# Optimization experiments

Measured on AMD Instinct MI355X. Metric: run time of the kernel, lower is better.

Reference implementation:

```python
import jax, jax.numpy as jnp
from jax import lax
import numpy as np


def _tv1d_row(y, lam):
    """Condat's direct O(n) 1D TV-L1 prox (TV1D_denoise) on one row.
    Solves min_x 0.5*||x-y||^2 + lam * sum|x_{i+1}-x_i|.
    State machine translation of Condat (2013) Algorithm 1.
    """
    W = y.shape[0]
    idx = jnp.arange(W)
    dt = y.dtype

    def write(out, lo, hi, v):
        # out[lo:hi+1] = v  (masked, jit-friendly)
        return jnp.where((idx >= lo) & (idx <= hi), v, out)

    def cond_fn(s):
        return ~s[9]

    def body_fn(s):
        out, k, k0, km, kp, umin, umax, vmin, vmax, done = s
        T = jnp.array(True)
        F = jnp.array(False)

        def branchA(_):  # k == W-1
            def a1(_):  # umin < 0: flush negative segment at vmin
                o = write(out, k0, km, vmin)
                k0n = km + 1
                vminn = y[jnp.minimum(k0n, W - 1)]
                return (o, k0n, k0n, k0n, kp, lam, vminn + lam - vmax, vminn, vmax, F)

            def a2(_):  # umax > 0: flush positive segment at vmax
                o = write(out, k0, kp, vmax)
                k0n = kp + 1
                vmaxn = y[jnp.minimum(k0n, W - 1)]
                return (o, k0n, k0n, km, k0n, vmaxn - lam - vmin, -lam, vmin, vmaxn, F)

            def a3(_):  # terminate
                v = vmin + umin / (k - k0 + 1).astype(dt)
                o = write(out, k0, k, v)
                return (o, k, k0, km, kp, umin, umax, v, vmax, T)

            return lax.cond(umin < 0, a1,
                            lambda _: lax.cond(umax > 0, a2, a3, None), None)

        def branchB(_):  # k < W-1
            yn = y[jnp.minimum(k + 1, W - 1)]
            umin_t = umin + yn - vmin
            umax_t = umax + yn - vmax

            def b1(_):  # negative jump: flush at vmin, restart
                o = write(out, k0, km, vmin)
                k0n = km + 1
                vminn = y[jnp.minimum(k0n, W - 1)]
                return (o, k0n, k0n, k0n, k0n, lam, -lam, vminn, vminn + 2 * lam, F)

            def b2(_):  # positive jump: flush at vmax, restart
                o = write(out, k0, kp, vmax)
                k0n = kp + 1
                vmaxn = y[jnp.minimum(k0n, W - 1)]
                return (o, k0n, k0n, k0n, k0n, lam, -lam, vmaxn - 2 * lam, vmaxn, F)

            def b3(_):  # extend current segment
                kn = k + 1
                denom = (kn - k0 + 1).astype(dt)
                hit_min = umin_t >= lam
                hit_max = umax_t <= -lam
                vminn = jnp.where(hit_min, vmin + (umin_t - lam) / denom, vmin)
                uminn = jnp.where(hit_min, lam, umin_t)
                kmn = jnp.where(hit_min, kn, km)
                vmaxn = jnp.where(hit_max, vmax + (umax_t + lam) / denom, vmax)
                umaxn = jnp.where(hit_max, -lam, umax_t)
                kpn = jnp.where(hit_max, kn, kp)
                return (out, kn, k0, kmn, kpn, uminn, umaxn, vminn, vmaxn, F)

            return lax.cond(umin_t < -lam, b1,
                            lambda _: lax.cond(umax_t > lam, b2, b3, None), None)

        return lax.cond(k == W - 1, branchA, branchB, None)

    z = jnp.int32(0)
    init = (jnp.zeros_like(y), z, z, z, z, lam, -lam, y[0] - lam, y[0] + lam, jnp.array(False))
    return lax.while_loop(cond_fn, body_fn, init)[0]


def tv1d_batch(y_flat, lam_rows):
    return jax.vmap(_tv1d_row)(y_flat, lam_rows)


def setup_inputs() -> dict:
    key = jax.random.key(0)
    N, C, H, W = 8, 3, 256, 512
    y = jax.random.normal(key, (N, C, H, W), dtype=jnp.float32)
    # learned lmbd parameter initialized so that softplus(lmbd) = 0.5 (lmbd_init=0.5, lmbd_zero<0 -> offset 0)
    lmbd = jnp.full((1, C), float(np.log(np.expm1(0.5))), dtype=jnp.float32)
    return {"y": y, "lmbd": lmbd}


def reference(y, lmbd):
    N, C, H, W = y.shape
    lam = jax.nn.softplus(lmbd)  # get_lmbd_val with lmbd_offset = 0
    lam_rows = jnp.broadcast_to(lam.reshape(1, C, 1), (N, C, H)).reshape(-1)  # (N*C*H,)
    x = tv1d_batch(y.reshape(-1, W), lam_rows)
    return x.reshape(N, C, H, W)
```

## Files before the change

kernel.cpp:

```cpp
#include <hip/hip_runtime.h>
#include <math.h>

#define TVW 512
#define TVH 256
#define TVC 3
#define WPB 2
#define BLOCK (WPB * 64)

__global__ __launch_bounds__(BLOCK)
void tv1d_condat_wave_kernel(const float* __restrict__ y,
                             const float* __restrict__ lmbd,
                             float* __restrict__ out,
                             int total_rows) {
    __shared__ __align__(16) float buf [WPB * TVW + 4];
    __shared__ __align__(16) float bneg[WPB * TVW + 4];
    __shared__ float rtab[520];
    const int tid  = threadIdx.x;
    const int wave = tid >> 6;
    const int lane = tid & 63;
    const bool hi  = lane >= 32;
    const int base_row = blockIdx.x * WPB;
    const int row = base_row + wave;

    {
        float4* b4 = (float4*)buf;
        float4* n4 = (float4*)bneg;
        const float4* s4 = (const float4*)(y + (size_t)base_row * TVW);
        #pragma unroll
        for (int i = 0; i < (WPB * TVW / 4); i += BLOCK) {
            const float4 v = s4[i + tid];
            b4[i + tid] = v;
            n4[i + tid] = make_float4(-v.x, -v.y, -v.z, -v.w);
        }
    }
    for (int i = tid; i < 520; i += BLOCK)
        rtab[i] = 1.0f / (float)(i == 0 ? 1 : i);
    if (tid < 4) {
        buf [WPB * TVW + tid] = 0.0f;
        bneg[WPB * TVW + tid] = 0.0f;
    }
    __syncthreads();

    if (row < total_rows) {
        const int c = (row / TVH) % TVC;
        float lam = log1pf(expf(lmbd[c]));
        lam = __uint_as_float(__builtin_amdgcn_readfirstlane(__float_as_uint(lam)));
        const float nlam   = -lam;
        const float twolam = 2.0f * lam;
        float* x = buf + wave * TVW;
        const float* xs = hi ? (bneg + wave * TVW) : (buf + wave * TVW);
        const float cneg = hi ? twolam : 0.0f;
        const float cpos = hi ? 0.0f : twolam;

        int k0 = 0, km = 0, kp = 0;
        float v = xs[0] - lam;
        float u = lam;
        float yn = xs[1];

        for (int guard = 0; guard < 4096; ++guard) {
            const int trips = (TVW - 1) - k0;
            float rn = 0.5f;
            const float* xpp = xs + (k0 + 2);
            const float* rpp = rtab + 3;
            const int kb = k0 + 1;

            unsigned long long jb = 0;
            int t = 0;
            for (; t < trips; ++t) {
                const float yn2 = xpp[t];
                const float rn2 = rpp[t];
                const float u_t = u + yn - v;
                jb = __ballot(u_t < nlam);
                if (jb) break;
                const unsigned long long cb = __ballot(u_t >= lam);
                const int kc = kb + t;
                km = (unsigned)(cb)       ? kc : km;
                kp = (unsigned)(cb >> 32) ? kc : kp;
                const float u_n = fminf(u_t, lam);
                v = fmaf(u_t - u_n, rn, v);
                u = u_n;
                yn = yn2; rn = rn2;
            }

            if (t < trips) {
                if ((unsigned)jb) {
                    const int k0n = km + 1;
                    const float fv  = __shfl(v, 0);
                    const float nvl = xs[k0n];
                    const float ynn = xs[k0n + 1];
                    for (int p = k0 + lane; p <= km; p += 64) x[p] = fv;
                    k0 = k0n; km = kp = k0n;
                    v = nvl - cneg;
                    yn = ynn;
                } else {
                    const int k0n = kp + 1;
                    const float fv  = -__shfl(v, 32);
                    const float nvl = xs[k0n];
                    const float ynn = xs[k0n + 1];
                    for (int p = k0 + lane; p <= kp; p += 64) x[p] = fv;
                    k0 = k0n; km = kp = k0n;
                    v = nvl - cpos;
                    yn = ynn;
                }
                u = lam;
            } else {
                const unsigned long long bb = __ballot(u < 0.0f);
                if ((unsigned)bb) {
                    const int k0n = km + 1;
                    const float fv = __shfl(v, 0);
                    float nvl = 0.0f, ynn = 0.0f;
                    if (k0n < TVW) { nvl = xs[k0n]; ynn = xs[k0n + 1]; }
                    const int pe = km < TVW - 1 ? km : TVW - 1;
                    for (int p = k0 + lane; p <= pe; p += 64) x[p] = fv;
                    if (k0n >= TVW) break;
                    const float tt = nvl - lam;
                    u = hi ? (tt - v) : lam;
                    v = hi ? v : nvl;
                    yn = ynn;
                    k0 = k0n; km = k0n;
                } else if ((unsigned)(bb >> 32)) {
                    const int k0n = kp + 1;
                    const float fv = -__shfl(v, 32);
                    float nvl = 0.0f, ynn = 0.0f;
                    if (k0n < TVW) { nvl = xs[k0n]; ynn = xs[k0n + 1]; }
                    const int pe = kp < TVW - 1 ? kp : TVW - 1;
                    for (int p = k0 + lane; p <= pe; p += 64) x[p] = fv;
                    if (k0n >= TVW) break;
                    const float tt = nvl - lam;
                    u = hi ? lam : (tt - v);
                    v = hi ? nvl : v;
                    yn = ynn;
                    k0 = k0n; kp = k0n;
                } else {
                    const float vt = fmaf(u, rtab[trips + 1], v);
                    const float fv = __shfl(vt, 0);
                    for (int p = k0 + lane; p < TVW; p += 64) x[p] = fv;
                    break;
                }
            }
        }
    }
    __syncthreads();

    {
        float4* b4 = (float4*)buf;
        float4* d4 = (float4*)(out + (size_t)base_row * TVW);
        #pragma unroll
        for (int i = 0; i < (WPB * TVW / 4); i += BLOCK)
            d4[i + tid] = b4[i + tid];
    }
}

extern "C" void kernel_launch(void* const* d_in, const int* in_sizes, int n_in,
                              void* d_out, int out_size, void* d_ws, size_t ws_size,
                              hipStream_t stream) {
    const float* y    = (const float*)d_in[0];
    const float* lmbd = (const float*)d_in[1];
    float* out = (float*)d_out;

    const int total_rows = in_sizes[0] / TVW;
    const int grid = (total_rows + WPB - 1) / WPB;
    tv1d_condat_wave_kernel<<<grid, BLOCK, 0, stream>>>(y, lmbd, out, total_rows);
}
```

Before: 276.0 us.

## Unroll Condat scan by four with register prefetch ring and rcp reciprocals

Replaces the per-step inner loop with a 4-way unrolled state machine that keeps a 12-element register ring (P/Q/R) of upcoming inputs, prefetched from LDS well ahead of use. Drops the shared reciprocal table in favour of hardware rcp approximations and compile-time constants for the first steps. Segment restarts reload the ring, and goto-based control flow replaces the nested loops. The aim is to hide LDS latency on the serial dependency chain and remove table loads. In exchange it adds register pressure, extra reloads at every jump, and approximate reciprocals.

```diff
diff --git a/kernel.cpp b/kernel.cpp
--- a/kernel.cpp
+++ b/kernel.cpp
@@ -6,15 +6,15 @@
 #define TVC 3
 #define WPB 2
 #define BLOCK (WPB * 64)
+#define PAD 12
 
 __global__ __launch_bounds__(BLOCK)
 void tv1d_condat_wave_kernel(const float* __restrict__ y,
                              const float* __restrict__ lmbd,
                              float* __restrict__ out,
                              int total_rows) {
-    __shared__ __align__(16) float buf [WPB * TVW + 4];
-    __shared__ __align__(16) float bneg[WPB * TVW + 4];
-    __shared__ float rtab[520];
+    __shared__ __align__(16) float buf [WPB * TVW + PAD];
+    __shared__ __align__(16) float bneg[WPB * TVW + PAD];
     const int tid  = threadIdx.x;
     const int wave = tid >> 6;
     const int lane = tid & 63;
@@ -33,9 +33,7 @@
             n4[i + tid] = make_float4(-v.x, -v.y, -v.z, -v.w);
         }
     }
-    for (int i = tid; i < 520; i += BLOCK)
-        rtab[i] = 1.0f / (float)(i == 0 ? 1 : i);
-    if (tid < 4) {
+    if (tid < PAD) {
         buf [WPB * TVW + tid] = 0.0f;
         bneg[WPB * TVW + tid] = 0.0f;
     }
@@ -52,93 +50,143 @@
         const float cneg = hi ? twolam : 0.0f;
         const float cpos = hi ? 0.0f : twolam;
 
-        int k0 = 0, km = 0, kp = 0;
-        float v = xs[0] - lam;
-        float u = lam;
-        float yn = xs[1];
-
-        for (int guard = 0; guard < 4096; ++guard) {
-            const int trips = (TVW - 1) - k0;
-            float rn = 0.5f;
-            const float* xpp = xs + (k0 + 2);
-            const float* rpp = rtab + 3;
-            const int kb = k0 + 1;
-
-            unsigned long long jb = 0;
-            int t = 0;
-            for (; t < trips; ++t) {
-                const float yn2 = xpp[t];
-                const float rn2 = rpp[t];
-                const float u_t = u + yn - v;
-                jb = __ballot(u_t < nlam);
-                if (jb) break;
-                const unsigned long long cb = __ballot(u_t >= lam);
-                const int kc = kb + t;
-                km = (unsigned)(cb)       ? kc : km;
-                kp = (unsigned)(cb >> 32) ? kc : kp;
-                const float u_n = fminf(u_t, lam);
-                v = fmaf(u_t - u_n, rn, v);
-                u = u_n;
-                yn = yn2; rn = rn2;
-            }
-
-            if (t < trips) {
-                if ((unsigned)jb) {
-                    const int k0n = km + 1;
-                    const float fv  = __shfl(v, 0);
-                    const float nvl = xs[k0n];
-                    const float ynn = xs[k0n + 1];
-                    for (int p = k0 + lane; p <= km; p += 64) x[p] = fv;
-                    k0 = k0n; km = kp = k0n;
-                    v = nvl - cneg;
-                    yn = ynn;
-                } else {
-                    const int k0n = kp + 1;
-                    const float fv  = -__shfl(v, 32);
-                    const float nvl = xs[k0n];
-                    const float ynn = xs[k0n + 1];
-                    for (int p = k0 + lane; p <= kp; p += 64) x[p] = fv;
-                    k0 = k0n; km = kp = k0n;
-                    v = nvl - cpos;
-                    yn = ynn;
-                }
-                u = lam;
-            } else {
-                const unsigned long long bb = __ballot(u < 0.0f);
-                if ((unsigned)bb) {
-                    const int k0n = km + 1;
-                    const float fv = __shfl(v, 0);
-                    float nvl = 0.0f, ynn = 0.0f;
-                    if (k0n < TVW) { nvl = xs[k0n]; ynn = xs[k0n + 1]; }
-                    const int pe = km < TVW - 1 ? km : TVW - 1;
-                    for (int p = k0 + lane; p <= pe; p += 64) x[p] = fv;
-                    if (k0n >= TVW) break;
-                    const float tt = nvl - lam;
-                    u = hi ? (tt - v) : lam;
-                    v = hi ? v : nvl;
-                    yn = ynn;
-                    k0 = k0n; km = k0n;
-                } else if ((unsigned)(bb >> 32)) {
-                    const int k0n = kp + 1;
-                    const float fv = -__shfl(v, 32);
-                    float nvl = 0.0f, ynn = 0.0f;
-                    if (k0n < TVW) { nvl = xs[k0n]; ynn = xs[k0n + 1]; }
-                    const int pe = kp < TVW - 1 ? kp : TVW - 1;
-                    for (int p = k0 + lane; p <= pe; p += 64) x[p] = fv;
-                    if (k0n >= TVW) break;
-                    const float tt = nvl - lam;
-                    u = hi ? lam : (tt - v);
-                    v = hi ? nvl : v;
-                    yn = ynn;
-                    k0 = k0n; kp = k0n;
-                } else {
-                    const float vt = fmaf(u, rtab[trips + 1], v);
-                    const float fv = __shfl(vt, 0);
-                    for (int p = k0 + lane; p < TVW; p += 64) x[p] = fv;
-                    break;
+        int k0, km, kp, t, trips, rem, seg_guard;
+        unsigned long long jb;
+        float u, v, nv, fv, tt, den_f;
+        float P0, P1, P2, P3, Q0, Q1, Q2, Q3, R0, R1, R2, R3, e0, e1, e2;
+        bool negj;
+
+        k0 = 0; km = 0; kp = 0; seg_guard = 2048; jb = 0;
+        v = xs[0] - lam;
+        u = lam;
+        P0 = xs[1];  P1 = xs[2];  P2 = xs[3];  P3 = xs[4];
+        Q0 = xs[5];  Q1 = xs[6];  Q2 = xs[7];  Q3 = xs[8];
+        R0 = xs[9];  R1 = xs[10]; R2 = xs[11]; R3 = xs[12];
+
+#define TVSTEP(EV, RN, KC) { \
+            const float u_t = u + (EV) - v; \
+            jb = __ballot(u_t < nlam);    \
+            if (jb) goto midjump; \
+            const unsigned long long cb = __ballot(u_t >= lam);  \
+            const int kc_ = (KC); \
+            km = (unsigned)(cb)       ? kc_ : km;    \
+            kp = (unsigned)(cb >> 32) ? kc_ : kp; \
+            const float u_n = fminf(u_t, lam); \
+            v = fmaf(u_t - u_n, (RN), v);   \
+            u = u_n; }
+
+#define TVPHASE(B0_, B1_, B2_, B3_) { \
+            den_f = (float)(t + 2); \
+            TVSTEP(B0_, __builtin_amdgcn_rcpf(den_f),        k0 + t + 1) \
+            TVSTEP(B1_, __builtin_amdgcn_rcpf(den_f + 1.0f), k0 + t + 2) \
+            TVSTEP(B2_, __builtin_amdgcn_rcpf(den_f + 2.0f), k0 + t + 3) \
+            TVSTEP(B3_, __builtin_amdgcn_rcpf(den_f + 3.0f), k0 + t + 4) \
+            B0_ = xs[k0 + t + 13]; B1_ = xs[k0 + t + 14]; \
+            B2_ = xs[k0 + t + 15]; B3_ = xs[k0 + t + 16]; \
+            t += 4; }
+
+seg_start:
+        if (--seg_guard < 0) goto done;
+        trips = (TVW - 1) - k0;
+        if (trips < 4) { t = 0; e0 = P0; e1 = P1; e2 = P2; goto rem_steps; }
+        TVSTEP(P0, 0.5f,           k0 + 1)
+        TVSTEP(P1, (1.0f / 3.0f),  k0 + 2)
+        TVSTEP(P2, 0.25f,          k0 + 3)
+        TVSTEP(P3, 0.2f,           k0 + 4)
+        P0 = xs[k0 + 13]; P1 = xs[k0 + 14]; P2 = xs[k0 + 15]; P3 = xs[k0 + 16];
+        if (trips < 8) { t = 4; e0 = Q0; e1 = Q1; e2 = Q2; goto rem_steps; }
+        TVSTEP(Q0, (1.0f / 6.0f),  k0 + 5)
+        TVSTEP(Q1, (1.0f / 7.0f),  k0 + 6)
+        TVSTEP(Q2, 0.125f,         k0 + 7)
+        TVSTEP(Q3, (1.0f / 9.0f),  k0 + 8)
+        Q0 = xs[k0 + 17]; Q1 = xs[k0 + 18]; Q2 = xs[k0 + 19]; Q3 = xs[k0 + 20];
+        t = 8;
+        for (;;) {
+            if (t + 4 > trips) { e0 = R0; e1 = R1; e2 = R2; break; }
+            TVPHASE(R0, R1, R2, R3)
+            if (t + 4 > trips) { e0 = P0; e1 = P1; e2 = P2; break; }
+            TVPHASE(P0, P1, P2, P3)
+            if (t + 4 > trips) { e0 = Q0; e1 = Q1; e2 = Q2; break; }
+            TVPHASE(Q0, Q1, Q2, Q3)
+        }
+rem_steps:
+        rem = trips - t;
+        if (rem > 0) {
+            den_f = (float)(t + 2);
+            TVSTEP(e0, __builtin_amdgcn_rcpf(den_f), k0 + t + 1)
+            if (rem > 1) {
+                TVSTEP(e1, __builtin_amdgcn_rcpf(den_f + 1.0f), k0 + t + 2)
+                if (rem > 2) {
+                    TVSTEP(e2, __builtin_amdgcn_rcpf(den_f + 2.0f), k0 + t + 3)
                 }
             }
         }
+
+        {
+            const unsigned long long bb = __ballot(u < 0.0f);
+            if ((unsigned)bb) {
+                const int k0n = km + 1;
+                fv = __shfl(v, 0);
+                if (k0n < TVW) {
+                    nv = xs[k0n];
+                    P0 = xs[k0n + 1];  P1 = xs[k0n + 2];  P2 = xs[k0n + 3];  P3 = xs[k0n + 4];
+                    Q0 = xs[k0n + 5];  Q1 = xs[k0n + 6];  Q2 = xs[k0n + 7];  Q3 = xs[k0n + 8];
+                    R0 = xs[k0n + 9];  R1 = xs[k0n + 10]; R2 = xs[k0n + 11]; R3 = xs[k0n + 12];
+                }
+                { const int pe = km < TVW - 1 ? km : TVW - 1;
+                  for (int p = k0 + lane; p <= pe; p += 64) x[p] = fv; }
+                if (k0n >= TVW) goto done;
+                tt = nv - lam;
+                u = hi ? (tt - v) : lam;
+                v = hi ? v : nv;
+                k0 = k0n; km = k0n;
+                goto seg_start;
+            } else if ((unsigned)(bb >> 32)) {
+                const int k0n = kp + 1;
+                fv = -__shfl(v, 32);
+                if (k0n < TVW) {
+                    nv = xs[k0n];
+                    P0 = xs[k0n + 1];  P1 = xs[k0n + 2];  P2 = xs[k0n + 3];  P3 = xs[k0n + 4];
+                    Q0 = xs[k0n + 5];  Q1 = xs[k0n + 6];  Q2 = xs[k0n + 7];  Q3 = xs[k0n + 8];
+                    R0 = xs[k0n + 9];  R1 = xs[k0n + 10]; R2 = xs[k0n + 11]; R3 = xs[k0n + 12];
+                }
+                { const int pe = kp < TVW - 1 ? kp : TVW - 1;
+                  for (int p = k0 + lane; p <= pe; p += 64) x[p] = fv; }
+                if (k0n >= TVW) goto done;
+                tt = nv - lam;
+                u = hi ? lam : (tt - v);
+                v = hi ? nv : v;
+                k0 = k0n; kp = k0n;
+                goto seg_start;
+            } else {
+                const float vt = fmaf(u, __builtin_amdgcn_rcpf((float)(trips + 1)), v);
+                fv = __shfl(vt, 0);
+                for (int p = k0 + lane; p < TVW; p += 64) x[p] = fv;
+                goto done;
+            }
+        }
+
+midjump:
+        {
+            negj = (unsigned)jb != 0;
+            const int fe = negj ? km : kp;
+            const int k0n = fe + 1;
+            const float b0  = __shfl(v, 0);
+            const float b32 = __shfl(v, 32);
+            fv = negj ? b0 : -b32;
+            nv = xs[k0n];
+            P0 = xs[k0n + 1];  P1 = xs[k0n + 2];  P2 = xs[k0n + 3];  P3 = xs[k0n + 4];
+            Q0 = xs[k0n + 5];  Q1 = xs[k0n + 6];  Q2 = xs[k0n + 7];  Q3 = xs[k0n + 8];
+            R0 = xs[k0n + 9];  R1 = xs[k0n + 10]; R2 = xs[k0n + 11]; R3 = xs[k0n + 12];
+            for (int p = k0 + lane; p <= fe; p += 64) x[p] = fv;
+            k0 = k0n; km = k0n; kp = k0n;
+            v = nv - (negj ? cneg : cpos);
+            u = lam;
+            goto seg_start;
+        }
+#undef TVPHASE
+#undef TVSTEP
+done:   ;
     }
     __syncthreads();
 
```

After: 245.1 us. 11.2% less time.
